# Kernel tuning notes

Measured on AMD Instinct MI355X. Metric: run time of the kernel, lower is better.

## Reference

```python
import jax, jax.numpy as jnp
import numpy as np

EPS = 1e-5

def layer_norm(x, w):
    mu = jnp.mean(x, axis=-1, keepdims=True)
    var = jnp.mean((x - mu) ** 2, axis=-1, keepdims=True)
    return (x - mu) * jax.lax.rsqrt(var + EPS) * w

def timestep_embedding(t, dim=256, max_period=10000.0):
    half = dim // 2
    freqs = jnp.exp(-np.log(max_period) * jnp.arange(half, dtype=jnp.float32) / half)
    args = t[:, None].astype(jnp.float32) * freqs[None]
    return jnp.concatenate([jnp.cos(args), jnp.sin(args)], axis=-1)  # (B, dim)


def setup_inputs() -> dict:
    key = jax.random.key(0)
    ks = jax.random.split(key, 16)
    B, S, D, H, L, V, C, F = 2, 1024, 768, 12, 12, 50258, 768, 256
    MLP = 4 * D
    w = 0.02  # init scale for weights
    return {
        "indices": jax.random.randint(ks[0], (B, S), 0, V, dtype=jnp.int32),
        "sigma": jax.random.uniform(ks[1], (B,), dtype=jnp.float32),
        "embed": jax.random.normal(ks[2], (V, D), jnp.float32) * w,
        "t_w1": jax.random.normal(ks[3], (C, F), jnp.float32) * w,
        "t_b1": jnp.zeros((C,), jnp.float32),
        "t_w2": jax.random.normal(ks[4], (C, C), jnp.float32) * w,
        "t_b2": jnp.zeros((C,), jnp.float32),
        "norm1_w": jnp.ones((L, D), jnp.float32),
        "qkv_w": jax.random.normal(ks[5], (L, 3 * D, D), jnp.float32) * w,
        "out_w": jax.random.normal(ks[6], (L, D, D), jnp.float32) * w,
        "norm2_w": jnp.ones((L, D), jnp.float32),
        "mlp_w1": jax.random.normal(ks[7], (L, MLP, D), jnp.float32) * w,
        "mlp_b1": jnp.zeros((L, MLP), jnp.float32),
        "mlp_w2": jax.random.normal(ks[8], (L, D, MLP), jnp.float32) * w,
        "mlp_b2": jnp.zeros((L, D), jnp.float32),
        "ada_w": jax.random.normal(ks[9], (L, 6 * D, C), jnp.float32) * w,
        "ada_b": jnp.zeros((L, 6 * D), jnp.float32),
        "normf_w": jnp.ones((D,), jnp.float32),
        "lin_w": jax.random.normal(ks[10], (V, D), jnp.float32) * w,
        "lin_b": jnp.zeros((V,), jnp.float32),
        "adaf_w": jax.random.normal(ks[11], (2 * D, C), jnp.float32) * w,
        "adaf_b": jnp.zeros((2 * D,), jnp.float32),
    }


def reference(indices, sigma, embed, t_w1, t_b1, t_w2, t_b2, norm1_w, qkv_w,
              out_w, norm2_w, mlp_w1, mlp_b1, mlp_w2, mlp_b2, ada_w, ada_b,
              normf_w, lin_w, lin_b, adaf_w, adaf_b):
    B, S = indices.shape
    D = embed.shape[1]
    L = qkv_w.shape[0]
    H = 12
    dh = D // H
    scale = 1.0 / np.sqrt(dh)

    x = embed[indices]  # (B, S, D)
    # conditioning: c = silu(MLP(sinusoidal(sigma)))
    tf = timestep_embedding(sigma)
    temb = jax.nn.silu(tf @ t_w1.T + t_b1) @ t_w2.T + t_b2
    c = jax.nn.silu(temb)  # (B, C)

    # NOTE: rotary cos/sin are computed but never applied in the original block.
    for l in range(L):
        ada = (c @ ada_w[l].T + ada_b[l]).reshape(B, 6, 1, D)
        sh_msa, sc_msa, g_msa = ada[:, 0], ada[:, 1], ada[:, 2]  # (B, 1, D)
        sh_mlp, sc_mlp, g_mlp = ada[:, 3], ada[:, 4], ada[:, 5]

        xm = layer_norm(x, norm1_w[l]) * (1 + sc_msa) + sh_msa
        qkv = (xm @ qkv_w[l].T).reshape(B, S, 3, H, dh)
        q, k, v = qkv[:, :, 0], qkv[:, :, 1], qkv[:, :, 2]  # (B, S, H, dh)
        attn = jnp.einsum('bqhd,bkhd->bhqk', q, k) * scale
        attn = jax.nn.softmax(attn, axis=-1)
        o = jnp.einsum('bhqk,bkhd->bqhd', attn, v).reshape(B, S, D)
        x = x + g_msa * (o @ out_w[l].T)

        xm = layer_norm(x, norm2_w[l]) * (1 + sc_mlp) + sh_mlp
        h = jax.nn.gelu(xm @ mlp_w1[l].T + mlp_b1[l], approximate=True)
        x = x + g_mlp * (h @ mlp_w2[l].T + mlp_b2[l])

    ada = (c @ adaf_w.T + adaf_b).reshape(B, 2, 1, D)
    shift, sc = ada[:, 0], ada[:, 1]
    xm = layer_norm(x, normf_w) * (1 + sc) + shift
    return xm @ lin_w.T + lin_b  # (B, S, V) log-scores
```

## Files before the change

### kernel.cpp

```cpp
#include <hip/hip_runtime.h>
#include <hip/hip_bf16.h>
#include <math.h>
#include <stdint.h>

typedef __hip_bfloat16 bf16;
typedef __attribute__((ext_vector_type(8))) short bf16x8;
typedef __attribute__((ext_vector_type(4))) float f32x4;

#define DEV_INLINE __device__ __forceinline__

DEV_INLINE float wred_sum(float v) {
    #pragma unroll
    for (int o = 32; o > 0; o >>= 1) v += __shfl_xor(v, o);
    return v;
}
DEV_INLINE float red16_max(float v) {
    v = fmaxf(v, __shfl_xor(v, 1)); v = fmaxf(v, __shfl_xor(v, 2));
    v = fmaxf(v, __shfl_xor(v, 4)); v = fmaxf(v, __shfl_xor(v, 8));
    return v;
}
DEV_INLINE float red16_sum(float v) {
    v += __shfl_xor(v, 1); v += __shfl_xor(v, 2);
    v += __shfl_xor(v, 4); v += __shfl_xor(v, 8);
    return v;
}
DEV_INLINE float gelu_tanh(float v) {
    float t = tanhf(0.7978845608028654f * (v + 0.044715f * v * v * v));
    return 0.5f * v * (1.f + t);
}
DEV_INLINE float silu(float v) { return v / (1.f + expf(-v)); }
DEV_INLINE short f2bs(float f) { bf16 h = __float2bfloat16(f); short s; __builtin_memcpy(&s, &h, 2); return s; }

typedef const __attribute__((address_space(1))) uint32_t* gptr_t;
typedef __attribute__((address_space(3))) uint32_t* lptr_t;

DEV_INLINE void gload_lds16(const bf16* gp, bf16* lp) {
    __builtin_amdgcn_global_load_lds((gptr_t)gp, (lptr_t)lp, 16, 0, 0);
}

#define WAITBAR4() asm volatile("s_waitcnt vmcnt(4)\ns_barrier" ::: "memory")
#define WAITBAR0() asm volatile("s_waitcnt vmcnt(0)\ns_barrier" ::: "memory")

DEV_INLINE int xcd_swz(int wg, int nwg) {
    int q = nwg >> 3, r = nwg & 7;
    int xcd = wg & 7, pos = wg >> 3;
    return (xcd < r ? xcd * (q + 1) : r * (q + 1) + (xcd - r) * q) + pos;
}

__global__ void cvt_bf16(const float* __restrict__ in, bf16* __restrict__ out, long n) {
    long i = ((long)blockIdx.x * blockDim.x + threadIdx.x) * 8;
    if (i >= n) return;
    float4 a = *(const float4*)(in + i);
    float4 b = *(const float4*)(in + i + 4);
    bf16x8 v;
    v[0] = f2bs(a.x); v[1] = f2bs(a.y); v[2] = f2bs(a.z); v[3] = f2bs(a.w);
    v[4] = f2bs(b.x); v[5] = f2bs(b.y); v[6] = f2bs(b.z); v[7] = f2bs(b.w);
    *(bf16x8*)(out + i) = v;
}

__global__ void embed_gather(const int* __restrict__ idx,
                             const float* __restrict__ embed,
                             float* __restrict__ x) {
    int i = blockIdx.x * blockDim.x + threadIdx.x;
    int m = i / 192, d4 = i % 192;
    ((float4*)x)[(size_t)m * 192 + d4] =
        ((const float4*)embed)[(size_t)idx[m] * 192 + d4];
}

__global__ void tstep_embed(const float* __restrict__ sigma, float* __restrict__ tf) {
    int t = threadIdx.x;
    int b = t >> 7, i = t & 127;
    float freq = expf(-9.210340371976184f * (float)i / 128.f);
    float a = sigma[b] * freq;
    tf[b * 256 + i]       = cosf(a);
    tf[b * 256 + 128 + i] = sinf(a);
}

template <int ACT>
__global__ void gemm_rowvec(const float* __restrict__ A, const float* __restrict__ W,
                            const float* __restrict__ bias, float* __restrict__ C,
                            int M, int N, int K) {
    int wid  = (int)((blockIdx.x * (size_t)blockDim.x + threadIdx.x) >> 6);
    int lane = threadIdx.x & 63;
    if (wid >= M * N) return;
    int m = wid / N, n = wid % N;
    const float* a = A + (size_t)m * K;
    const float* w = W + (size_t)n * K;
    float s = 0.f;
    for (int k = lane; k < K; k += 64) s = fmaf(a[k], w[k], s);
    s = wred_sum(s);
    if (lane == 0) {
        if (bias) s += bias[n];
        if (ACT == 2) s = silu(s);
        C[wid] = s;
    }
}

__global__ void ada_all(const float* __restrict__ c, const float* __restrict__ ada_w,
                        const float* __restrict__ ada_b, float* __restrict__ out) {
    const int C = 768, SIXD = 4608, B = 2;
    int wid  = (int)((blockIdx.x * (size_t)blockDim.x + threadIdx.x) >> 6);
    int lane = threadIdx.x & 63;
    if (wid >= 12 * B * SIXD) return;
    int j = wid % SIXD;
    int lb = wid / SIXD;
    int b = lb % B, l = lb / B;
    const float* a = c + (size_t)b * C;
    const float* w = ada_w + ((size_t)l * SIXD + j) * C;
    float s = 0.f;
    for (int k = lane; k < C; k += 64) s = fmaf(a[k], w[k], s);
    s = wred_sum(s);
    if (lane == 0) out[wid] = s + ada_b[l * SIXD + j];
}

__global__ __launch_bounds__(256) void ln_mod(const float* __restrict__ x,
                                              const float* __restrict__ w,
                                              const float* __restrict__ sc,
                                              const float* __restrict__ sh,
                                              int bstride,
                                              bf16* __restrict__ out) {
    int r = blockIdx.x;
    int b = r >> 10;
    const float* xr = x + (size_t)r * 768;
    int tid = threadIdx.x, lane = tid & 63, wv = tid >> 6;
    float v0 = xr[tid], v1 = xr[tid + 256], v2 = xr[tid + 512];
    __shared__ float redA[4], redB[4];
    float s = wred_sum(v0 + v1 + v2);
    if (lane == 0) redA[wv] = s;
    __syncthreads();
    float mu = (redA[0] + redA[1] + redA[2] + redA[3]) * (1.f / 768.f);
    float d0 = v0 - mu, d1 = v1 - mu, d2 = v2 - mu;
    float vs = wred_sum(d0 * d0 + d1 * d1 + d2 * d2);
    if (lane == 0) redB[wv] = vs;
    __syncthreads();
    float var  = (redB[0] + redB[1] + redB[2] + redB[3]) * (1.f / 768.f);
    float rstd = rsqrtf(var + 1e-5f);
    const float* scb = sc + (size_t)b * bstride;
    const float* shb = sh + (size_t)b * bstride;
    bf16* outr = out + (size_t)r * 768;
    outr[tid]       = __float2bfloat16(d0 * rstd * w[tid]       * (1.f + scb[tid])       + shb[tid]);
    outr[tid + 256] = __float2bfloat16(d1 * rstd * w[tid + 256] * (1.f + scb[tid + 256]) + shb[tid + 256]);
    outr[tid + 512] = __float2bfloat16(d2 * rstd * w[tid + 512] * (1.f + scb[tid + 512]) + shb[tid + 512]);
}

template <int NPART>
__global__ __launch_bounds__(256) void ln_mod_red(float* __restrict__ x,
                                                  const float* __restrict__ part,
                                                  const float* __restrict__ bias,
                                                  const float* __restrict__ gate,
                                                  int gst,
                                                  const float* __restrict__ w,
                                                  const float* __restrict__ sc,
                                                  const float* __restrict__ sh,
                                                  int bstride,
                                                  bf16* __restrict__ out) {
    const size_t PST = (size_t)2048 * 768;
    int r = blockIdx.x;
    int b = r >> 10;
    float* xr = x + (size_t)r * 768;
    int tid = threadIdx.x, lane = tid & 63, wv = tid >> 6;

    float v[3];
    #pragma unroll
    for (int e = 0; e < 3; e++) {
        int d = tid + e * 256;
        float s0 = 0.f;
        #pragma unroll
        for (int p = 0; p < NPART; p++) s0 += part[(size_t)p * PST + (size_t)r * 768 + d];
        if (bias) s0 += bias[d];
        v[e] = xr[d] + gate[b * gst + d] * s0;
        xr[d] = v[e];
    }

    __shared__ float redA[4], redB[4];
    float s = wred_sum(v[0] + v[1] + v[2]);
    if (lane == 0) redA[wv] = s;
    __syncthreads();
    float mu = (redA[0] + redA[1] + redA[2] + redA[3]) * (1.f / 768.f);
    float d0 = v[0] - mu, d1 = v[1] - mu, d2 = v[2] - mu;
    float vs = wred_sum(d0 * d0 + d1 * d1 + d2 * d2);
    if (lane == 0) redB[wv] = vs;
    __syncthreads();
    float var  = (redB[0] + redB[1] + redB[2] + redB[3]) * (1.f / 768.f);
    float rstd = rsqrtf(var + 1e-5f);
    const float* scb = sc + (size_t)b * bstride;
    const float* shb = sh + (size_t)b * bstride;
    bf16* outr = out + (size_t)r * 768;
    outr[tid]       = __float2bfloat16(d0 * rstd * w[tid]       * (1.f + scb[tid])       + shb[tid]);
    outr[tid + 256] = __float2bfloat16(d1 * rstd * w[tid + 256] * (1.f + scb[tid + 256]) + shb[tid + 256]);
    outr[tid + 512] = __float2bfloat16(d2 * rstd * w[tid + 512] * (1.f + scb[tid + 512]) + shb[tid + 512]);
}

template <int ACT, int OMODE, int SK>
__global__ __launch_bounds__(256) void gemm_mfma(const bf16* __restrict__ A,
                                                 const bf16* __restrict__ W,
                                                 const float* __restrict__ bias,
                                                 void* __restrict__ Cout,
                                                 bf16* __restrict__ vtout,
                                                 int M, int N, int K) {
    __shared__ __align__(16) bf16 SHB[6 * 128 * 32];
    int tid = threadIdx.x;
    int w = tid >> 6, l = tid & 63;
    int l16 = l & 15, g = l >> 4;
    int wgid = xcd_swz(blockIdx.x, gridDim.x);
    int MT = M >> 7;
    int nt = gridDim.x / (MT * SK);
    int m0 = (wgid % MT) * 128;
    int n  = (wgid / MT) % nt;
    int s  = wgid / (MT * nt);
    int n0 = n * 128;
    int kb = K / SK;
    int k0 = s * kb;
    int wr = (w >> 1) * 64, wc = (w & 1) * 64;

    f32x4 acc[4][4];
    f32x4 zero4 = {0.f, 0.f, 0.f, 0.f};
    #pragma unroll
    for (int i = 0; i < 4; i++)
        #pragma unroll
        for (int j = 0; j < 4; j++) acc[i][j] = zero4;

    int srow = w * 32 + (l >> 2);
    int scol = ((l & 3) ^ ((l >> 3) & 3)) * 8;
    const bf16* gA0 = A + (size_t)(m0 + srow) * K + k0 + scol;
    const bf16* gA1 = gA0 + (size_t)16 * K;
    int nr0 = n0 + srow;      if (nr0 > N - 1) nr0 = N - 1;
    int nr1 = n0 + srow + 16; if (nr1 > N - 1) nr1 = N - 1;
    const bf16* gW0 = W + (size_t)nr0 * K + k0 + scol;
    const bf16* gW1 = W + (size_t)nr1 * K + k0 + scol;
    int ldsA0 = (w * 32) * 32, ldsA1 = (w * 32 + 16) * 32;

    int sA = (g ^ ((l16 >> 1) & 3)) * 8;

    auto SAp = [&](int bufi) { return &SHB[bufi * 4096]; };
    auto SWp = [&](int bufi) { return &SHB[(3 + bufi) * 4096]; };

    auto STAGE = [&](int kk, int bufi) {
        gload_lds16(gA0 + kk, SAp(bufi) + ldsA0);
        gload_lds16(gA1 + kk, SAp(bufi) + ldsA1);
        gload_lds16(gW0 + kk, SWp(bufi) + ldsA0);
        gload_lds16(gW1 + kk, SWp(bufi) + ldsA1);
    };

    int KT = kb >> 5;
    STAGE(0, 0);
    if (KT > 1) STAGE(32, 1);

    for (int k = 0; k < KT; ++k) {
        if (k == KT - 1) { WAITBAR0(); } else { WAITBAR4(); }
        if (k + 2 < KT) STAGE((k + 2) * 32, (k + 2) % 3);
        int cbuf = k % 3;
        const bf16* sa = SAp(cbuf);
        const bf16* sw = SWp(cbuf);
        bf16x8 af[4], bfr[4];
        #pragma unroll
        for (int mi = 0; mi < 4; mi++)
            af[mi] = *(const bf16x8*)&sa[(wr + mi * 16 + l16) * 32 + sA];
        #pragma unroll
        for (int ni = 0; ni < 4; ni++)
            bfr[ni] = *(const bf16x8*)&sw[(wc + ni * 16 + l16) * 32 + sA];
        #pragma unroll
        for (int mi = 0; mi < 4; mi++)
            #pragma unroll
            for (int ni = 0; ni < 4; ni++)
                acc[mi][ni] = __builtin_amdgcn_mfma_f32_16x16x32_bf16(
                    af[mi], bfr[ni], acc[mi][ni], 0, 0, 0);
    }

    if (OMODE == 0) {
        float* Lf = (float*)SHB;
        #pragma unroll
        for (int h = 0; h < 2; ++h) {
            __syncthreads();
            if ((w >> 1) == h) {
                #pragma unroll
                for (int ni = 0; ni < 4; ni++) {
                    int lc = wc + ni * 16 + l16;
                    int colg = n0 + lc;
                    float bv = (bias && colg < N) ? bias[colg] : 0.f;
                    #pragma unroll
                    for (int mi = 0; mi < 4; mi++) {
                        int lr = (wr - h * 64) + mi * 16 + g * 4;
                        #pragma unroll
                        for (int jj = 0; jj < 4; jj++)
                            Lf[(lr + jj) * 132 + lc] = acc[mi][ni][jj] + bv;
                    }
                }
            }
            __syncthreads();
            #pragma unroll
            for (int pass = 0; pass < 8; ++pass) {
                int row = pass * 8 + w * 2 + (l >> 5);
                int c4  = (l & 31) * 4;
                const float* src = &Lf[row * 132 + c4];
                float* dst = (float*)Cout + (size_t)(m0 + h * 64 + row) * N + n0 + c4;
                int col = n0 + c4;
                if (col + 3 < N) {
                    *(float2*)dst       = *(const float2*)src;
                    *(float2*)(dst + 2) = *(const float2*)(src + 2);
                } else {
                    #pragma unroll
                    for (int e = 0; e < 4; ++e)
                        if (col + e < N) dst[e] = src[e];
                }
            }
        }
        return;
    }
    if (OMODE == 3 && n0 >= 1536) {
        #pragma unroll
        for (int ni = 0; ni < 4; ni++) {
            int cv = n0 + wc + ni * 16 + l16 - 1536;
            int h = cv >> 6, d = cv & 63;
            #pragma unroll
            for (int mi = 0; mi < 4; mi++) {
                int row = m0 + wr + mi * 16 + g * 4;
                int b = row >> 10, ss = row & 1023;
                short4 pk;
                pk.x = f2bs(acc[mi][ni][0]); pk.y = f2bs(acc[mi][ni][1]);
                pk.z = f2bs(acc[mi][ni][2]); pk.w = f2bs(acc[mi][ni][3]);
                *(short4*)&vtout[(((size_t)(b * 12 + h) * 64 + d)) * 1024 + ss] = pk;
            }
        }
        return;
    }
    float* pout = (OMODE == 4) ? (float*)Cout + (size_t)s * M * N : (float*)Cout;
    #pragma unroll
    for (int ni = 0; ni < 4; ni++) {
        int col = n0 + wc + ni * 16 + l16;
        if (col >= N) continue;
        float bv = (OMODE != 4 && bias) ? bias[col] : 0.f;
        #pragma unroll
        for (int mi = 0; mi < 4; mi++) {
            #pragma unroll
            for (int jj = 0; jj < 4; jj++) {
                int row = m0 + wr + mi * 16 + g * 4 + jj;
                float v = acc[mi][ni][jj] + bv;
                if (ACT == 1) v = gelu_tanh(v);
                if (OMODE == 1 || OMODE == 3) {
                    ((bf16*)Cout)[(size_t)row * N + col] = __float2bfloat16(v);
                } else {
                    pout[(size_t)row * N + col] = v;
                }
            }
        }
    }
}

__global__ __launch_bounds__(256) void attn_mfma(const bf16* __restrict__ qkv,
                                                 const bf16* __restrict__ vt,
                                                 bf16* __restrict__ ao) {
    const int S = 1024, C3 = 2304;
    int wgid = xcd_swz(blockIdx.x, gridDim.x);
    int bh = wgid >> 4, b = bh / 12, h = bh % 12;
    int q0 = (wgid & 15) * 64;
    int tid = threadIdx.x, w = tid >> 6, l = tid & 63;
    int l16 = l & 15, g = l >> 4;

    __shared__ __align__(16) bf16 Ks[3][64 * 64];
    __shared__ __align__(16) bf16 Vs[3][64 * 64];
    __shared__ __align__(16) bf16 Ps[4][16 * 72];

    const size_t qbase = ((size_t)(b * S + q0 + w * 16 + l16)) * C3 + h * 64;
    bf16x8 qf[2];
    qf[0] = *(const bf16x8*)&qkv[qbase + g * 8];
    qf[1] = *(const bf16x8*)&qkv[qbase + 32 + g * 8];

    f32x4 o_acc[4];
    f32x4 zero4 = {0.f, 0.f, 0.f, 0.f};
    #pragma unroll
    for (int ni = 0; ni < 4; ni++) o_acc[ni] = zero4;
    float mrow[4] = {-1e30f, -1e30f, -1e30f, -1e30f};
    float lrow[4] = {0.f, 0.f, 0.f, 0.f};
    const float cscale = 0.125f * 1.44269504088896f;

    int sr0 = w * 16 + (l >> 3);
    int sr1 = sr0 + 8;
    int cb  = (l & 7) * 16;
    int sc0 = (cb ^ ((sr0 & 7) << 4)) >> 1;
    int sc1 = (cb ^ ((sr1 & 7) << 4)) >> 1;
    const bf16* gk0 = qkv + ((size_t)(b * S) + sr0) * C3 + 768 + h * 64 + sc0;
    const bf16* gk1 = qkv + ((size_t)(b * S) + sr1) * C3 + 768 + h * 64 + sc1;
    const bf16* gv0 = vt + ((size_t)bh * 64 + sr0) * 1024 + sc0;
    const bf16* gv1 = vt + ((size_t)bh * 64 + sr1) * 1024 + sc1;
    int ldk0 = (w * 16) * 64, ldk1 = (w * 16 + 8) * 64;

    auto STAGEKV = [&](int t, int bufi) {
        gload_lds16(gk0 + (size_t)(t * 64) * C3, &Ks[bufi][ldk0]);
        gload_lds16(gk1 + (size_t)(t * 64) * C3, &Ks[bufi][ldk1]);
        gload_lds16(gv0 + t * 64, &Vs[bufi][ldk0]);
        gload_lds16(gv1 + t * 64, &Vs[bufi][ldk1]);
    };

    STAGEKV(0, 0);
    STAGEKV(1, 1);

    for (int it = 0; it < 16; ++it) {
        if (it == 15) { WAITBAR0(); } else { WAITBAR4(); }
        if (it + 2 < 16) STAGEKV(it + 2, (it + 2) % 3);
        int cur = it % 3;

        f32x4 sfrag[4];
        #pragma unroll
        for (int kf = 0; kf < 4; kf++) {
            sfrag[kf] = zero4;
            int key = kf * 16 + l16;
            #pragma unroll
            for (int kc = 0; kc < 2; kc++) {
                int byteoff = key * 128 + (((kc * 32 + g * 8) * 2) ^ ((key & 7) << 4));
                bf16x8 kb = *(const bf16x8*)((const char*)Ks[cur] + byteoff);
                sfrag[kf] = __builtin_amdgcn_mfma_f32_16x16x32_bf16(qf[kc], kb, sfrag[kf], 0, 0, 0);
            }
        }

        float pv[4][4];
        #pragma unroll
        for (int j = 0; j < 4; j++) {
            float t0 = sfrag[0][j] * cscale, t1 = sfrag[1][j] * cscale;
            float t2 = sfrag[2][j] * cscale, t3 = sfrag[3][j] * cscale;
            float mx = fmaxf(fmaxf(t0, t1), fmaxf(t2, t3));
            mx = red16_max(mx);
            float mnew = fmaxf(mrow[j], mx);
            float r = exp2f(mrow[j] - mnew);
            mrow[j] = mnew;
            float p0 = exp2f(t0 - mnew), p1 = exp2f(t1 - mnew);
            float p2 = exp2f(t2 - mnew), p3 = exp2f(t3 - mnew);
            pv[0][j] = p0; pv[1][j] = p1; pv[2][j] = p2; pv[3][j] = p3;
            float ps = red16_sum(p0 + p1 + p2 + p3);
            lrow[j] = lrow[j] * r + ps;
            #pragma unroll
            for (int ni = 0; ni < 4; ni++) o_acc[ni][j] *= r;
        }

        #pragma unroll
        for (int kf = 0; kf < 4; kf++)
            #pragma unroll
            for (int j = 0; j < 4; j++)
                Ps[w][(g * 4 + j) * 72 + kf * 16 + l16] = __float2bfloat16(pv[kf][j]);

        #pragma unroll
        for (int kc = 0; kc < 2; kc++) {
            bf16x8 pa = *(const bf16x8*)&Ps[w][l16 * 72 + kc * 32 + g * 8];
            #pragma unroll
            for (int ni = 0; ni < 4; ni++) {
                int d = ni * 16 + l16;
                int byteoff = d * 128 + (((kc * 32 + g * 8) * 2) ^ ((d & 7) << 4));
                bf16x8 vb = *(const bf16x8*)((const char*)Vs[cur] + byteoff);
                o_acc[ni] = __builtin_amdgcn_mfma_f32_16x16x32_bf16(pa, vb, o_acc[ni], 0, 0, 0);
            }
        }
    }

    float linv[4];
    #pragma unroll
    for (int j = 0; j < 4; j++) linv[j] = 1.f / lrow[j];
    #pragma unroll
    for (int ni = 0; ni < 4; ni++) {
        #pragma unroll
        for (int jj = 0; jj < 4; jj++) {
            int row = q0 + w * 16 + g * 4 + jj;
            ao[((size_t)(b * S + row)) * 768 + h * 64 + ni * 16 + l16] =
                __float2bfloat16(o_acc[ni][jj] * linv[jj]);
        }
    }
}

extern "C" void kernel_launch(void* const* d_in, const int* in_sizes, int n_in,
                              void* d_out, int out_size, void* d_ws, size_t ws_size,
                              hipStream_t stream) {
    const int B = 2, S = 1024, D = 768, L = 12, V = 50258, C = 768, F = 256, MLP = 3072;
    const int M = B * S;

    const int*   indices = (const int*)d_in[0];
    const float* sigma   = (const float*)d_in[1];
    const float* embed   = (const float*)d_in[2];
    const float* t_w1    = (const float*)d_in[3];
    const float* t_b1    = (const float*)d_in[4];
    const float* t_w2    = (const float*)d_in[5];
    const float* t_b2    = (const float*)d_in[6];
    const float* norm1_w = (const float*)d_in[7];
    const float* qkv_w   = (const float*)d_in[8];
    const float* out_w   = (const float*)d_in[9];
    const float* norm2_w = (const float*)d_in[10];
    const float* mlp_w1  = (const float*)d_in[11];
    const float* mlp_b1  = (const float*)d_in[12];
    const float* mlp_w2  = (const float*)d_in[13];
    const float* mlp_b2  = (const float*)d_in[14];
    const float* ada_w   = (const float*)d_in[15];
    const float* ada_b   = (const float*)d_in[16];
    const float* normf_w = (const float*)d_in[17];
    const float* lin_w   = (const float*)d_in[18];
    const float* lin_b   = (const float*)d_in[19];
    const float* adaf_w  = (const float*)d_in[20];
    const float* adaf_b  = (const float*)d_in[21];

    char* p = (char*)d_ws;
    auto alloc = [&](size_t bytes) { char* r = p; p += (bytes + 255) & ~(size_t)255; return r; };

    float* x     = (float*)alloc((size_t)M * D * 4);
    bf16*  xm    = (bf16*) alloc((size_t)M * D * 2);
    bf16*  qkvb  = (bf16*) alloc((size_t)M * 3 * D * 2);
    bf16*  aob   = (bf16*) alloc((size_t)M * D * 2);
    bf16*  hbb   = (bf16*) alloc((size_t)M * MLP * 2);
    bf16*  vtb   = (bf16*) alloc((size_t)24 * 64 * 1024 * 2);
    float* partb = (float*)alloc((size_t)4 * M * D * 4);
    bf16*  linb  = (bf16*) alloc((size_t)V * D * 2);
    float* tf    = (float*)alloc((size_t)B * F * 4);
    float* h1    = (float*)alloc((size_t)B * C * 4);
    float* cb    = (float*)alloc((size_t)B * C * 4);
    float* ada   = (float*)alloc((size_t)L * B * 6 * D * 4);
    float* adaf  = (float*)alloc((size_t)B * 2 * D * 4);

    const size_t n_qkvw = (size_t)L * 2304 * 768;
    const size_t n_outw = (size_t)L * 768 * 768;
    const size_t n_w1   = (size_t)L * 3072 * 768;
    const size_t n_w2   = (size_t)L * 768 * 3072;
    const size_t per_layer = (size_t)(2304 + 768 + 3072 + 3072) * 768;
    size_t used = (size_t)(p - (char*)d_ws);
    bool all_w = (ws_size - used) >= ((n_qkvw + n_outw + n_w1 + n_w2) * 2 + 1024);

    bf16 *wqkv, *wout, *ww1, *ww2;
    if (all_w) {
        wqkv = (bf16*)alloc(n_qkvw * 2);
        wout = (bf16*)alloc(n_outw * 2);
        ww1  = (bf16*)alloc(n_w1 * 2);
        ww2  = (bf16*)alloc(n_w2 * 2);
    } else {
        bf16* wl = (bf16*)alloc(per_layer * 2);
        wqkv = wl;
        wout = wqkv + (size_t)2304 * 768;
        ww1  = wout + (size_t)768 * 768;
        ww2  = ww1 + (size_t)3072 * 768;
    }

    auto cgrid = [](long n) { return (unsigned)((n / 8 + 255) / 256); };
    dim3 blk(256);

    embed_gather<<<(M * 192) / 256, blk, 0, stream>>>(indices, embed, x);
    tstep_embed<<<1, blk, 0, stream>>>(sigma, tf);
    gemm_rowvec<2><<<(B * C * 64) / 256, blk, 0, stream>>>(tf, t_w1, t_b1, h1, B, C, F);
    gemm_rowvec<2><<<(B * C * 64) / 256, blk, 0, stream>>>(h1, t_w2, t_b2, cb, B, C, C);
    ada_all<<<(L * B * 6 * D * 64) / 256, blk, 0, stream>>>(cb, ada_w, ada_b, ada);
    gemm_rowvec<0><<<(B * 2 * D * 64) / 256, blk, 0, stream>>>(cb, adaf_w, adaf_b, adaf, B, 2 * D, C);
    cvt_bf16<<<cgrid((long)V * D), blk, 0, stream>>>(lin_w, linb, (long)V * D);
    if (all_w) {
        cvt_bf16<<<cgrid((long)n_qkvw), blk, 0, stream>>>(qkv_w, wqkv, (long)n_qkvw);
        cvt_bf16<<<cgrid((long)n_outw), blk, 0, stream>>>(out_w, wout, (long)n_outw);
        cvt_bf16<<<cgrid((long)n_w1),   blk, 0, stream>>>(mlp_w1, ww1, (long)n_w1);
        cvt_bf16<<<cgrid((long)n_w2),   blk, 0, stream>>>(mlp_w2, ww2, (long)n_w2);
    }

    const int MT = M / 128;
    for (int l = 0; l < L; l++) {
        const float* adaL = ada + (size_t)l * B * 6 * D;
        bf16 *wq, *wo, *w1, *w2;
        if (all_w) {
            wq = wqkv + (size_t)l * 2304 * 768;
            wo = wout + (size_t)l * 768 * 768;
            w1 = ww1 + (size_t)l * 3072 * 768;
            w2 = ww2 + (size_t)l * 768 * 3072;
        } else {
            wq = wqkv; wo = wout; w1 = ww1; w2 = ww2;
            cvt_bf16<<<cgrid((long)2304 * 768), blk, 0, stream>>>(qkv_w + (size_t)l * 2304 * 768, wq, (long)2304 * 768);
            cvt_bf16<<<cgrid((long)768 * 768),  blk, 0, stream>>>(out_w + (size_t)l * 768 * 768,  wo, (long)768 * 768);
            cvt_bf16<<<cgrid((long)3072 * 768), blk, 0, stream>>>(mlp_w1 + (size_t)l * 3072 * 768, w1, (long)3072 * 768);
            cvt_bf16<<<cgrid((long)768 * 3072), blk, 0, stream>>>(mlp_w2 + (size_t)l * 768 * 3072, w2, (long)768 * 3072);
        }

        if (l == 0) {
            ln_mod<<<M, blk, 0, stream>>>(x, norm1_w, adaL + D, adaL, 6 * D, xm);
        } else {
            const float* adaP = ada + (size_t)(l - 1) * B * 6 * D;
            ln_mod_red<4><<<M, blk, 0, stream>>>(
                x, partb, mlp_b2 + (size_t)(l - 1) * D, adaP + 5 * D, 6 * D,
                norm1_w + (size_t)l * D, adaL + D, adaL, 6 * D, xm);
        }

        gemm_mfma<0, 3, 1><<<MT * (2304 / 128), blk, 0, stream>>>(
            xm, wq, nullptr, qkvb, vtb, M, 2304, 768);
        attn_mfma<<<384, blk, 0, stream>>>(qkvb, vtb, aob);
        gemm_mfma<0, 4, 2><<<MT * (768 / 128) * 2, blk, 0, stream>>>(
            aob, wo, nullptr, partb, nullptr, M, 768, 768);
        ln_mod_red<2><<<M, blk, 0, stream>>>(
            x, partb, nullptr, adaL + 2 * D, 6 * D,
            norm2_w + (size_t)l * D, adaL + 4 * D, adaL + 3 * D, 6 * D, xm);

        gemm_mfma<1, 1, 1><<<MT * (3072 / 128), blk, 0, stream>>>(
            xm, w1, mlp_b1 + (size_t)l * MLP, hbb, nullptr, M, 3072, 768);
        gemm_mfma<0, 4, 4><<<MT * (768 / 128) * 4, blk, 0, stream>>>(
            hbb, w2, nullptr, partb, nullptr, M, 768, 3072);
    }

    {
        const float* adaP = ada + (size_t)(L - 1) * B * 6 * D;
        ln_mod_red<4><<<M, blk, 0, stream>>>(
            x, partb, mlp_b2 + (size_t)(L - 1) * D, adaP + 5 * D, 6 * D,
            normf_w, adaf + D, adaf, 2 * D, xm);
    }
    gemm_mfma<0, 0, 1><<<MT * ((V + 127) / 128), blk, 0, stream>>>(
        xm, linb, lin_b, (float*)d_out, nullptr, M, V, 768);
}
```

Measured before the change: 2.095 ms.

## Add 256-row GEMM tile variant for MLP down-proj and final vocab projection

Templates the MFMA GEMM on MI, the number of 16-row m-fragments per wave, so a block can cover 256 rows instead of 128. It uses the 256-row tile for the vocab logits GEMM and for the MLP second GEMM, which also moves from split-K 4 to split-K 8. The split-K partial buffer and the reduction in the following layernorm are widened to match. The larger tile halves how often the huge vocab weight matrix is re-read per row tile, at the cost of more accumulator registers, more LDS and a heavier split-K reduction.

```diff
diff --git a/kernel.cpp b/kernel.cpp
--- a/kernel.cpp
+++ b/kernel.cpp
@@ -38,6 +38,7 @@
     __builtin_amdgcn_global_load_lds((gptr_t)gp, (lptr_t)lp, 16, 0, 0);
 }
 
+#define WAITBAR6() asm volatile("s_waitcnt vmcnt(6)\ns_barrier" ::: "memory")
 #define WAITBAR4() asm volatile("s_waitcnt vmcnt(4)\ns_barrier" ::: "memory")
 #define WAITBAR0() asm volatile("s_waitcnt vmcnt(0)\ns_barrier" ::: "memory")
 
@@ -191,55 +192,61 @@
     outr[tid + 512] = __float2bfloat16(d2 * rstd * w[tid + 512] * (1.f + scb[tid + 512]) + shb[tid + 512]);
 }
 
-template <int ACT, int OMODE, int SK>
+template <int ACT, int OMODE, int SK, int MI>
 __global__ __launch_bounds__(256) void gemm_mfma(const bf16* __restrict__ A,
                                                  const bf16* __restrict__ W,
                                                  const float* __restrict__ bias,
                                                  void* __restrict__ Cout,
                                                  bf16* __restrict__ vtout,
                                                  int M, int N, int K) {
-    __shared__ __align__(16) bf16 SHB[6 * 128 * 32];
+    constexpr int BM = MI * 32;
+    constexpr int EA = BM / 64;
+    __shared__ __align__(16) bf16 SHB[3 * BM * 32 + 3 * 4096];
     int tid = threadIdx.x;
     int w = tid >> 6, l = tid & 63;
     int l16 = l & 15, g = l >> 4;
     int wgid = xcd_swz(blockIdx.x, gridDim.x);
-    int MT = M >> 7;
+    int MT = M / BM;
     int nt = gridDim.x / (MT * SK);
-    int m0 = (wgid % MT) * 128;
+    int m0 = (wgid % MT) * BM;
     int n  = (wgid / MT) % nt;
     int s  = wgid / (MT * nt);
     int n0 = n * 128;
     int kb = K / SK;
     int k0 = s * kb;
-    int wr = (w >> 1) * 64, wc = (w & 1) * 64;
-
-    f32x4 acc[4][4];
+    int wr = (w >> 1) * (BM / 2), wc = (w & 1) * 64;
+
+    f32x4 acc[MI][4];
     f32x4 zero4 = {0.f, 0.f, 0.f, 0.f};
     #pragma unroll
-    for (int i = 0; i < 4; i++)
+    for (int i = 0; i < MI; i++)
         #pragma unroll
         for (int j = 0; j < 4; j++) acc[i][j] = zero4;
 
-    int srow = w * 32 + (l >> 2);
+    int srowA = w * (BM / 4) + (l >> 2);
+    int srowW = w * 32 + (l >> 2);
     int scol = ((l & 3) ^ ((l >> 3) & 3)) * 8;
-    const bf16* gA0 = A + (size_t)(m0 + srow) * K + k0 + scol;
-    const bf16* gA1 = gA0 + (size_t)16 * K;
-    int nr0 = n0 + srow;      if (nr0 > N - 1) nr0 = N - 1;
-    int nr1 = n0 + srow + 16; if (nr1 > N - 1) nr1 = N - 1;
+    const bf16* gA = A + (size_t)(m0 + srowA) * K + k0 + scol;
+    int nr0 = n0 + srowW;      if (nr0 > N - 1) nr0 = N - 1;
+    int nr1 = n0 + srowW + 16; if (nr1 > N - 1) nr1 = N - 1;
     const bf16* gW0 = W + (size_t)nr0 * K + k0 + scol;
     const bf16* gW1 = W + (size_t)nr1 * K + k0 + scol;
-    int ldsA0 = (w * 32) * 32, ldsA1 = (w * 32 + 16) * 32;
+    int ldsA = (w * (BM / 4)) * 32;
+    int ldsW0 = (w * 32) * 32, ldsW1 = (w * 32 + 16) * 32;
 
     int sA = (g ^ ((l16 >> 1) & 3)) * 8;
 
-    auto SAp = [&](int bufi) { return &SHB[bufi * 4096]; };
-    auto SWp = [&](int bufi) { return &SHB[(3 + bufi) * 4096]; };
+    bf16* SAb = SHB;
+    bf16* SWb = SHB + 3 * BM * 32;
+    auto SAp = [&](int bufi) { return SAb + bufi * (BM * 32); };
+    auto SWp = [&](int bufi) { return SWb + bufi * 4096; };
 
     auto STAGE = [&](int kk, int bufi) {
-        gload_lds16(gA0 + kk, SAp(bufi) + ldsA0);
-        gload_lds16(gA1 + kk, SAp(bufi) + ldsA1);
-        gload_lds16(gW0 + kk, SWp(bufi) + ldsA0);
-        gload_lds16(gW1 + kk, SWp(bufi) + ldsA1);
+        #pragma unroll
+        for (int e = 0; e < EA; e++)
+            gload_lds16(gA + (size_t)e * 16 * K + kk, SAp(bufi) + ldsA + e * 16 * 32);
+        gload_lds16(gW0 + kk, SWp(bufi) + ldsW0);
+        gload_lds16(gW1 + kk, SWp(bufi) + ldsW1);
     };
 
     int KT = kb >> 5;
@@ -247,20 +254,22 @@
     if (KT > 1) STAGE(32, 1);
 
     for (int k = 0; k < KT; ++k) {
-        if (k == KT - 1) { WAITBAR0(); } else { WAITBAR4(); }
+        if (k == KT - 1) { WAITBAR0(); }
+        else if (MI == 8) { WAITBAR6(); }
+        else { WAITBAR4(); }
         if (k + 2 < KT) STAGE((k + 2) * 32, (k + 2) % 3);
         int cbuf = k % 3;
         const bf16* sa = SAp(cbuf);
         const bf16* sw = SWp(cbuf);
-        bf16x8 af[4], bfr[4];
-        #pragma unroll
-        for (int mi = 0; mi < 4; mi++)
+        bf16x8 af[MI], bfr[4];
+        #pragma unroll
+        for (int mi = 0; mi < MI; mi++)
             af[mi] = *(const bf16x8*)&sa[(wr + mi * 16 + l16) * 32 + sA];
         #pragma unroll
         for (int ni = 0; ni < 4; ni++)
             bfr[ni] = *(const bf16x8*)&sw[(wc + ni * 16 + l16) * 32 + sA];
         #pragma unroll
-        for (int mi = 0; mi < 4; mi++)
+        for (int mi = 0; mi < MI; mi++)
             #pragma unroll
             for (int ni = 0; ni < 4; ni++)
                 acc[mi][ni] = __builtin_amdgcn_mfma_f32_16x16x32_bf16(
@@ -270,17 +279,19 @@
     if (OMODE == 0) {
         float* Lf = (float*)SHB;
         #pragma unroll
-        for (int h = 0; h < 2; ++h) {
+        for (int h = 0; h < BM / 64; ++h) {
             __syncthreads();
-            if ((w >> 1) == h) {
+            int hw  = (MI == 4) ? h : (h >> 1);
+            int mi0 = (MI == 4) ? 0 : (h & 1) * 4;
+            if ((w >> 1) == hw) {
                 #pragma unroll
                 for (int ni = 0; ni < 4; ni++) {
                     int lc = wc + ni * 16 + l16;
                     int colg = n0 + lc;
                     float bv = (bias && colg < N) ? bias[colg] : 0.f;
                     #pragma unroll
-                    for (int mi = 0; mi < 4; mi++) {
-                        int lr = (wr - h * 64) + mi * 16 + g * 4;
+                    for (int mi = mi0; mi < mi0 + 4; mi++) {
+                        int lr = (mi - mi0) * 16 + g * 4;
                         #pragma unroll
                         for (int jj = 0; jj < 4; jj++)
                             Lf[(lr + jj) * 132 + lc] = acc[mi][ni][jj] + bv;
@@ -313,7 +324,7 @@
             int cv = n0 + wc + ni * 16 + l16 - 1536;
             int h = cv >> 6, d = cv & 63;
             #pragma unroll
-            for (int mi = 0; mi < 4; mi++) {
+            for (int mi = 0; mi < MI; mi++) {
                 int row = m0 + wr + mi * 16 + g * 4;
                 int b = row >> 10, ss = row & 1023;
                 short4 pk;
@@ -331,7 +342,7 @@
         if (col >= N) continue;
         float bv = (OMODE != 4 && bias) ? bias[col] : 0.f;
         #pragma unroll
-        for (int mi = 0; mi < 4; mi++) {
+        for (int mi = 0; mi < MI; mi++) {
             #pragma unroll
             for (int jj = 0; jj < 4; jj++) {
                 int row = m0 + wr + mi * 16 + g * 4 + jj;
@@ -503,7 +514,7 @@
     bf16*  aob   = (bf16*) alloc((size_t)M * D * 2);
     bf16*  hbb   = (bf16*) alloc((size_t)M * MLP * 2);
     bf16*  vtb   = (bf16*) alloc((size_t)24 * 64 * 1024 * 2);
-    float* partb = (float*)alloc((size_t)4 * M * D * 4);
+    float* partb = (float*)alloc((size_t)8 * M * D * 4);
     bf16*  linb  = (bf16*) alloc((size_t)V * D * 2);
     float* tf    = (float*)alloc((size_t)B * F * 4);
     float* h1    = (float*)alloc((size_t)B * C * 4);
@@ -551,6 +562,7 @@
     }
 
     const int MT = M / 128;
+    const int MT8 = M / 256;
     for (int l = 0; l < L; l++) {
         const float* adaL = ada + (size_t)l * B * 6 * D;
         bf16 *wq, *wo, *w1, *w2;
@@ -571,32 +583,32 @@
             ln_mod<<<M, blk, 0, stream>>>(x, norm1_w, adaL + D, adaL, 6 * D, xm);
         } else {
             const float* adaP = ada + (size_t)(l - 1) * B * 6 * D;
-            ln_mod_red<4><<<M, blk, 0, stream>>>(
+            ln_mod_red<8><<<M, blk, 0, stream>>>(
                 x, partb, mlp_b2 + (size_t)(l - 1) * D, adaP + 5 * D, 6 * D,
                 norm1_w + (size_t)l * D, adaL + D, adaL, 6 * D, xm);
         }
 
-        gemm_mfma<0, 3, 1><<<MT * (2304 / 128), blk, 0, stream>>>(
+        gemm_mfma<0, 3, 1, 4><<<MT * (2304 / 128), blk, 0, stream>>>(
             xm, wq, nullptr, qkvb, vtb, M, 2304, 768);
         attn_mfma<<<384, blk, 0, stream>>>(qkvb, vtb, aob);
-        gemm_mfma<0, 4, 2><<<MT * (768 / 128) * 2, blk, 0, stream>>>(
+        gemm_mfma<0, 4, 2, 4><<<MT * (768 / 128) * 2, blk, 0, stream>>>(
             aob, wo, nullptr, partb, nullptr, M, 768, 768);
         ln_mod_red<2><<<M, blk, 0, stream>>>(
             x, partb, nullptr, adaL + 2 * D, 6 * D,
             norm2_w + (size_t)l * D, adaL + 4 * D, adaL + 3 * D, 6 * D, xm);
 
-        gemm_mfma<1, 1, 1><<<MT * (3072 / 128), blk, 0, stream>>>(
+        gemm_mfma<1, 1, 1, 4><<<MT * (3072 / 128), blk, 0, stream>>>(
             xm, w1, mlp_b1 + (size_t)l * MLP, hbb, nullptr, M, 3072, 768);
-        gemm_mfma<0, 4, 4><<<MT * (768 / 128) * 4, blk, 0, stream>>>(
+        gemm_mfma<0, 4, 8, 8><<<MT8 * (768 / 128) * 8, blk, 0, stream>>>(
             hbb, w2, nullptr, partb, nullptr, M, 768, 3072);
     }
 
     {
         const float* adaP = ada + (size_t)(L - 1) * B * 6 * D;
-        ln_mod_red<4><<<M, blk, 0, stream>>>(
+        ln_mod_red<8><<<M, blk, 0, stream>>>(
             x, partb, mlp_b2 + (size_t)(L - 1) * D, adaP + 5 * D, 6 * D,
             normf_w, adaf + D, adaf, 2 * D, xm);
     }
-    gemm_mfma<0, 0, 1><<<MT * ((V + 127) / 128), blk, 0, stream>>>(
+    gemm_mfma<0, 0, 1, 8><<<MT8 * ((V + 127) / 128), blk, 0, stream>>>(
         xm, linb, lin_b, (float*)d_out, nullptr, M, V, 768);
 }
```

After: 2.280 ms. 1.09x slower.

## Add dedicated 256x256-tile vocab projection GEMM with 512-thread blocks

Applied to the files above, without the earlier changes.

Replaces the generic 128x128 GEMM for the final vocabulary projection with a new kernel using 256x256 output tiles, 8 waves, and a triple-buffered LDS pipeline, keeping the LDS-staged coalesced fp32 store epilogue. The larger tile roughly doubles operand reuse per loaded byte on the largest GEMM, which writes a big fp32 logits tensor. The old OMODE==0 epilogue is removed from the generic kernel and the STAGE lambda is inlined. The change trades higher register and LDS use per block (lower occupancy, 96KB LDS) for fewer blocks and less global traffic.

```diff
diff --git a/kernel.cpp b/kernel.cpp
--- a/kernel.cpp
+++ b/kernel.cpp
@@ -229,26 +229,32 @@
     const bf16* gW0 = W + (size_t)nr0 * K + k0 + scol;
     const bf16* gW1 = W + (size_t)nr1 * K + k0 + scol;
     int ldsA0 = (w * 32) * 32, ldsA1 = (w * 32 + 16) * 32;
-
     int sA = (g ^ ((l16 >> 1) & 3)) * 8;
 
     auto SAp = [&](int bufi) { return &SHB[bufi * 4096]; };
     auto SWp = [&](int bufi) { return &SHB[(3 + bufi) * 4096]; };
 
-    auto STAGE = [&](int kk, int bufi) {
-        gload_lds16(gA0 + kk, SAp(bufi) + ldsA0);
-        gload_lds16(gA1 + kk, SAp(bufi) + ldsA1);
-        gload_lds16(gW0 + kk, SWp(bufi) + ldsA0);
-        gload_lds16(gW1 + kk, SWp(bufi) + ldsA1);
-    };
-
     int KT = kb >> 5;
-    STAGE(0, 0);
-    if (KT > 1) STAGE(32, 1);
+    gload_lds16(gA0 + 0, SAp(0) + ldsA0);
+    gload_lds16(gA1 + 0, SAp(0) + ldsA1);
+    gload_lds16(gW0 + 0, SWp(0) + ldsA0);
+    gload_lds16(gW1 + 0, SWp(0) + ldsA1);
+    if (KT > 1) {
+        gload_lds16(gA0 + 32, SAp(1) + ldsA0);
+        gload_lds16(gA1 + 32, SAp(1) + ldsA1);
+        gload_lds16(gW0 + 32, SWp(1) + ldsA0);
+        gload_lds16(gW1 + 32, SWp(1) + ldsA1);
+    }
 
     for (int k = 0; k < KT; ++k) {
         if (k == KT - 1) { WAITBAR0(); } else { WAITBAR4(); }
-        if (k + 2 < KT) STAGE((k + 2) * 32, (k + 2) % 3);
+        if (k + 2 < KT) {
+            int bufi = (k + 2) % 3, kk = (k + 2) * 32;
+            gload_lds16(gA0 + kk, SAp(bufi) + ldsA0);
+            gload_lds16(gA1 + kk, SAp(bufi) + ldsA1);
+            gload_lds16(gW0 + kk, SWp(bufi) + ldsA0);
+            gload_lds16(gW1 + kk, SWp(bufi) + ldsA1);
+        }
         int cbuf = k % 3;
         const bf16* sa = SAp(cbuf);
         const bf16* sw = SWp(cbuf);
@@ -267,46 +273,6 @@
                     af[mi], bfr[ni], acc[mi][ni], 0, 0, 0);
     }
 
-    if (OMODE == 0) {
-        float* Lf = (float*)SHB;
-        #pragma unroll
-        for (int h = 0; h < 2; ++h) {
-            __syncthreads();
-            if ((w >> 1) == h) {
-                #pragma unroll
-                for (int ni = 0; ni < 4; ni++) {
-                    int lc = wc + ni * 16 + l16;
-                    int colg = n0 + lc;
-                    float bv = (bias && colg < N) ? bias[colg] : 0.f;
-                    #pragma unroll
-                    for (int mi = 0; mi < 4; mi++) {
-                        int lr = (wr - h * 64) + mi * 16 + g * 4;
-                        #pragma unroll
-                        for (int jj = 0; jj < 4; jj++)
-                            Lf[(lr + jj) * 132 + lc] = acc[mi][ni][jj] + bv;
-                    }
-                }
-            }
-            __syncthreads();
-            #pragma unroll
-            for (int pass = 0; pass < 8; ++pass) {
-                int row = pass * 8 + w * 2 + (l >> 5);
-                int c4  = (l & 31) * 4;
-                const float* src = &Lf[row * 132 + c4];
-                float* dst = (float*)Cout + (size_t)(m0 + h * 64 + row) * N + n0 + c4;
-                int col = n0 + c4;
-                if (col + 3 < N) {
-                    *(float2*)dst       = *(const float2*)src;
-                    *(float2*)(dst + 2) = *(const float2*)(src + 2);
-                } else {
-                    #pragma unroll
-                    for (int e = 0; e < 4; ++e)
-                        if (col + e < N) dst[e] = src[e];
-                }
-            }
-        }
-        return;
-    }
     if (OMODE == 3 && n0 >= 1536) {
         #pragma unroll
         for (int ni = 0; ni < 4; ni++) {
@@ -342,6 +308,118 @@
                 } else {
                     pout[(size_t)row * N + col] = v;
                 }
+            }
+        }
+    }
+}
+
+__global__ __launch_bounds__(512) void gemm_vocab(const bf16* __restrict__ A,
+                                                  const bf16* __restrict__ W,
+                                                  const float* __restrict__ bias,
+                                                  float* __restrict__ Cout,
+                                                  int M, int N, int K) {
+    __shared__ __align__(16) bf16 SHB[49152];
+    int tid = threadIdx.x;
+    int w = tid >> 6, l = tid & 63;
+    int l16 = l & 15, g = l >> 4;
+    int wm = w >> 2, wn = w & 3;
+    int wgid = xcd_swz(blockIdx.x, gridDim.x);
+    int MT = M >> 8;
+    int m0 = (wgid % MT) * 256;
+    int n0 = (wgid / MT) * 256;
+
+    f32x4 acc[8][4];
+    f32x4 zero4 = {0.f, 0.f, 0.f, 0.f};
+    #pragma unroll
+    for (int i = 0; i < 8; i++)
+        #pragma unroll
+        for (int j = 0; j < 4; j++) acc[i][j] = zero4;
+
+    int srow = w * 16 + (l >> 2);
+    int scol = ((l & 3) ^ ((l >> 3) & 3)) * 8;
+    const bf16* gA0 = A + (size_t)(m0 + srow) * K + scol;
+    const bf16* gA1 = gA0 + (size_t)128 * K;
+    int nb0 = n0 + srow;       if (nb0 > N - 1) nb0 = N - 1;
+    int nb1 = n0 + 128 + srow; if (nb1 > N - 1) nb1 = N - 1;
+    const bf16* gB0 = W + (size_t)nb0 * K + scol;
+    const bf16* gB1 = W + (size_t)nb1 * K + scol;
+    int ldw = (w * 16) * 32;
+    int sA = (g ^ ((l16 >> 1) & 3)) * 8;
+
+    auto SAp = [&](int bufi) { return &SHB[bufi * 8192]; };
+    auto SBp = [&](int bufi) { return &SHB[24576 + bufi * 8192]; };
+
+    int KT = K >> 5;
+    #pragma unroll
+    for (int t = 0; t < 2; ++t) {
+        gload_lds16(gA0 + t * 32, SAp(t) + ldw);
+        gload_lds16(gA1 + t * 32, SAp(t) + 4096 + ldw);
+        gload_lds16(gB0 + t * 32, SBp(t) + ldw);
+        gload_lds16(gB1 + t * 32, SBp(t) + 4096 + ldw);
+    }
+
+    for (int k = 0; k < KT; ++k) {
+        if (k == KT - 1) { WAITBAR0(); } else { WAITBAR4(); }
+        if (k + 2 < KT) {
+            int bufi = (k + 2) % 3, kk = (k + 2) * 32;
+            gload_lds16(gA0 + kk, SAp(bufi) + ldw);
+            gload_lds16(gA1 + kk, SAp(bufi) + 4096 + ldw);
+            gload_lds16(gB0 + kk, SBp(bufi) + ldw);
+            gload_lds16(gB1 + kk, SBp(bufi) + 4096 + ldw);
+        }
+        int cbuf = k % 3;
+        const bf16* sa = SAp(cbuf);
+        const bf16* sb = SBp(cbuf);
+        bf16x8 af[8], bfr[4];
+        #pragma unroll
+        for (int mi = 0; mi < 8; mi++)
+            af[mi] = *(const bf16x8*)&sa[(wm * 128 + mi * 16 + l16) * 32 + sA];
+        #pragma unroll
+        for (int ni = 0; ni < 4; ni++)
+            bfr[ni] = *(const bf16x8*)&sb[(wn * 64 + ni * 16 + l16) * 32 + sA];
+        #pragma unroll
+        for (int mi = 0; mi < 8; mi++)
+            #pragma unroll
+            for (int ni = 0; ni < 4; ni++)
+                acc[mi][ni] = __builtin_amdgcn_mfma_f32_16x16x32_bf16(
+                    af[mi], bfr[ni], acc[mi][ni], 0, 0, 0);
+    }
+
+    float* Lf = (float*)SHB;
+    #pragma unroll
+    for (int h = 0; h < 4; ++h) {
+        __syncthreads();
+        if (wm == (h >> 1)) {
+            int mi0 = (h & 1) * 4;
+            #pragma unroll
+            for (int ni = 0; ni < 4; ni++) {
+                int lc = wn * 64 + ni * 16 + l16;
+                int colg = n0 + lc;
+                float bv = (bias && colg < N) ? bias[colg] : 0.f;
+                #pragma unroll
+                for (int mi2 = 0; mi2 < 4; mi2++) {
+                    int lr = mi2 * 16 + g * 4;
+                    #pragma unroll
+                    for (int jj = 0; jj < 4; jj++)
+                        Lf[(lr + jj) * 260 + lc] = acc[mi0 + mi2][ni][jj] + bv;
+                }
+            }
+        }
+        __syncthreads();
+        #pragma unroll
+        for (int pass = 0; pass < 8; ++pass) {
+            int row = pass * 8 + (tid >> 6);
+            int c4  = (tid & 63) * 4;
+            const float* src = &Lf[row * 260 + c4];
+            float* dst = Cout + (size_t)(m0 + h * 64 + row) * N + n0 + c4;
+            int col = n0 + c4;
+            if (col + 3 < N) {
+                *(float2*)dst       = *(const float2*)src;
+                *(float2*)(dst + 2) = *(const float2*)(src + 2);
+            } else {
+                #pragma unroll
+                for (int e = 0; e < 4; ++e)
+                    if (col + e < N) dst[e] = src[e];
             }
         }
     }
@@ -597,6 +675,6 @@
             x, partb, mlp_b2 + (size_t)(L - 1) * D, adaP + 5 * D, 6 * D,
             normf_w, adaf + D, adaf, 2 * D, xm);
     }
-    gemm_mfma<0, 0, 1><<<MT * ((V + 127) / 128), blk, 0, stream>>>(
-        xm, linb, lin_b, (float*)d_out, nullptr, M, V, 768);
-}
+    gemm_vocab<<<(M / 256) * ((V + 255) / 256), dim3(512), 0, stream>>>(
+        xm, linb, lin_b, (float*)d_out, M, V, 768);
+}
```

Result: no change. 2.083 ms, median of 2 (-0.6%).
